# Optimization experiments

Hardware: AMD Instinct MI355X
Metric: run time of the kernel (lower is better)

## Reference

```python
import jax, jax.numpy as jnp
import numpy as np

N = 100000
E = 1600000
F = 128
H = 8
D = F // H
NC = 3


def setup_inputs() -> dict:
    key = jax.random.key(0)
    ks = jax.random.split(key, 12)
    s = lambda fan_in: 1.0 / np.sqrt(fan_in)
    x = jax.random.normal(ks[0], (N, F), dtype=jnp.float32)
    edge_index = jax.random.randint(ks[1], (2, E), 0, N, dtype=jnp.int64)
    edge_attr = jax.random.normal(ks[2], (E, 2), dtype=jnp.float32)
    # params stored as [in, out] so y = x @ W + b
    Wqkv = jax.random.uniform(ks[3], (F, 3 * F), jnp.float32, -s(F), s(F))
    Wedge = jax.random.uniform(ks[4], (2, H), jnp.float32, -s(2), s(2))
    Wout = jax.random.uniform(ks[5], (F, F), jnp.float32, -s(F), s(F))
    bout = jax.random.uniform(ks[6], (F,), jnp.float32, -s(F), s(F))
    ln_w = jnp.ones((F,), jnp.float32)
    ln_b = jnp.zeros((F,), jnp.float32)
    Wc1 = jax.random.uniform(ks[7], (F, F // 2), jnp.float32, -s(F), s(F))
    bc1 = jax.random.uniform(ks[8], (F // 2,), jnp.float32, -s(F), s(F))
    Wc2 = jax.random.uniform(ks[9], (F // 2, NC), jnp.float32, -s(F // 2), s(F // 2))
    bc2 = jax.random.uniform(ks[10], (NC,), jnp.float32, -s(F // 2), s(F // 2))
    return {"x": x, "edge_index": edge_index, "edge_attr": edge_attr,
            "Wqkv": Wqkv, "Wedge": Wedge, "Wout": Wout, "bout": bout,
            "ln_w": ln_w, "ln_b": ln_b,
            "Wc1": Wc1, "bc1": bc1, "Wc2": Wc2, "bc2": bc2}


def reference(x, edge_index, edge_attr, Wqkv, Wedge, Wout, bout,
              ln_w, ln_b, Wc1, bc1, Wc2, bc2):
    n = x.shape[0]
    scale = D ** (-0.5)
    qkv = x @ Wqkv                                # [N, 3F]
    q, k, v = [t.reshape(n, H, D) for t in jnp.split(qkv, 3, axis=-1)]
    src = edge_index[0]   # j (source / neighbor)
    dst = edge_index[1]   # i (target, softmax segment)
    edge_bias = edge_attr @ Wedge                 # [E, H]
    # per-edge biased attention score
    score = jnp.einsum('ehd,ehd->eh', q[dst], k[src]) * scale + edge_bias
    # segment softmax over incoming edges of each target node
    m = jax.lax.stop_gradient(jax.ops.segment_max(score, dst, num_segments=n))
    ex = jnp.exp(score - m[dst])
    denom = jax.ops.segment_sum(ex, dst, num_segments=n) + 1e-16
    w = ex / denom[dst]                           # [E, H]
    agg = jax.ops.segment_sum(v[src] * w[..., None], dst, num_segments=n)
    attn_out = agg.reshape(n, F) @ Wout + bout    # to_out
    h = x + attn_out
    mu = jnp.mean(h, axis=-1, keepdims=True)
    var = jnp.mean((h - mu) ** 2, axis=-1, keepdims=True)
    h = (h - mu) / jnp.sqrt(var + 1e-5) * ln_w + ln_b
    h = jax.nn.relu(h @ Wc1 + bc1)
    return h @ Wc2 + bc2
```

## Files before the change

kernel.cpp:

```cpp
#include <hip/hip_runtime.h>
#include <stdint.h>

#define N_NODES 100000
#define N_EDGES 1600000
#define FDIM 128
#define NH 8
#define NCLS 3

static constexpr float SCALE = 0.25f;

typedef _Float16 f16x8 __attribute__((ext_vector_type(8)));
typedef _Float16 f16x4 __attribute__((ext_vector_type(4)));
typedef float    f32x4 __attribute__((ext_vector_type(4)));

__global__ __launch_bounds__(256) void k_hist(const int* __restrict__ ei,
                                              int* __restrict__ cnt) {
    int e = blockIdx.x * 256 + threadIdx.x;
    if (e < N_EDGES) {
        int d = ei[N_EDGES + e];
        atomicAdd(&cnt[d], 1);
    }
}

__global__ __launch_bounds__(256) void k_scan1(const int* __restrict__ cnt,
                                               int* __restrict__ bsum) {
    __shared__ int sd[256];
    int t = threadIdx.x;
    int i0 = blockIdx.x * 1024 + t * 4;
    int s = 0;
#pragma unroll
    for (int j = 0; j < 4; ++j) {
        int i = i0 + j;
        if (i < N_NODES) s += cnt[i];
    }
    sd[t] = s;
    __syncthreads();
    for (int off = 128; off > 0; off >>= 1) {
        if (t < off) sd[t] += sd[t + off];
        __syncthreads();
    }
    if (t == 0) bsum[blockIdx.x] = sd[0];
}

__global__ __launch_bounds__(128) void k_scan2(const int* __restrict__ bsum,
                                               int* __restrict__ boff,
                                               int* __restrict__ row_start) {
    __shared__ int sd[128];
    int t = threadIdx.x;
    int v = (t < 98) ? bsum[t] : 0;
    sd[t] = v;
    __syncthreads();
    for (int off = 1; off < 128; off <<= 1) {
        int add = (t >= off) ? sd[t - off] : 0;
        __syncthreads();
        sd[t] += add;
        __syncthreads();
    }
    if (t < 98) boff[t] = sd[t] - v;
    if (t == 0) row_start[N_NODES] = N_EDGES;
}

__global__ __launch_bounds__(256) void k_scan3(const int* __restrict__ cnt,
                                               const int* __restrict__ boff,
                                               int* __restrict__ row_start,
                                               int* __restrict__ cursor) {
    __shared__ int sd[256];
    int t = threadIdx.x;
    int i0 = blockIdx.x * 1024 + t * 4;
    int c[4];
    int s = 0;
#pragma unroll
    for (int j = 0; j < 4; ++j) {
        int i = i0 + j;
        c[j] = (i < N_NODES) ? cnt[i] : 0;
        s += c[j];
    }
    sd[t] = s;
    __syncthreads();
    for (int off = 1; off < 256; off <<= 1) {
        int add = (t >= off) ? sd[t - off] : 0;
        __syncthreads();
        sd[t] += add;
        __syncthreads();
    }
    int run = boff[blockIdx.x] + sd[t] - s;
#pragma unroll
    for (int j = 0; j < 4; ++j) {
        int i = i0 + j;
        if (i < N_NODES) { row_start[i] = run; cursor[i] = run; }
        run += c[j];
    }
}

__global__ __launch_bounds__(256) void k_scatter(const int* __restrict__ ei,
                                                 const float* __restrict__ ea,
                                                 int* __restrict__ cursor,
                                                 float4* __restrict__ se4) {
    int e = blockIdx.x * 256 + threadIdx.x;
    if (e < N_EDGES) {
        int s = ei[e];
        int d = ei[N_EDGES + e];
        float2 a = *(const float2*)(ea + (long)e * 2);
        int pos = atomicAdd(&cursor[d], 1);
        se4[pos] = make_float4(__int_as_float(s), a.x, a.y, 0.0f);
    }
}

__global__ __launch_bounds__(256) void k_cvt(const float* __restrict__ x,
                                             const float* __restrict__ Wqkv,
                                             const float* __restrict__ Wout,
                                             _Float16* __restrict__ x_h,
                                             _Float16* __restrict__ Wqkv_t,
                                             _Float16* __restrict__ Wout_t) {
    long i = (long)blockIdx.x * 256 + threadIdx.x;
    float4 v = ((const float4*)x)[i];
    f16x4 h = { (_Float16)v.x, (_Float16)v.y, (_Float16)v.z, (_Float16)v.w };
    *(f16x4*)(x_h + i * 4) = h;
    if (i < 128 * 384) {
        int k = (int)(i / 384), n = (int)(i % 384);
        Wqkv_t[(long)n * 128 + k] = (_Float16)Wqkv[i];
    }
    if (i < 128 * 128) {
        int k = (int)(i / 128), n = (int)(i % 128);
        Wout_t[(long)n * 128 + k] = (_Float16)Wout[i];
    }
}

__global__ __launch_bounds__(256) void k_mm_qkv(const _Float16* __restrict__ x_h,
                                                const _Float16* __restrict__ Wt,
                                                float* __restrict__ q_tab,
                                                _Float16* __restrict__ kv_h) {
    int wave = threadIdx.x >> 6, l = threadIdx.x & 63;
    int row0 = blockIdx.x * 64 + wave * 16;
    int lr = l & 15, lg = l >> 4;
    int arow = row0 + lr;
    bool aok = arow < N_NODES;
    long abase = (long)arow * 128 + lg * 8;

    f32x4 acc[24];
#pragma unroll
    for (int c = 0; c < 24; ++c) acc[c] = (f32x4){0.f, 0.f, 0.f, 0.f};

#pragma unroll
    for (int kk = 0; kk < 4; ++kk) {
        f16x8 a = aok ? *(const f16x8*)(x_h + abase + kk * 32) : (f16x8){};
        const _Float16* wb = Wt + (long)lr * 128 + lg * 8 + kk * 32;
#pragma unroll
        for (int c = 0; c < 24; ++c) {
            f16x8 b = *(const f16x8*)(wb + (long)c * 16 * 128);
            acc[c] = __builtin_amdgcn_mfma_f32_16x16x32_f16(a, b, acc[c], 0, 0, 0);
        }
    }

    int orow_base = row0 + lg * 4;
#pragma unroll
    for (int c = 0; c < 24; ++c) {
#pragma unroll
        for (int j = 0; j < 4; ++j) {
            int orow = orow_base + j;
            if (orow < N_NODES) {
                float v = acc[c][j];
                if (c < 8)       q_tab[(long)orow * 128 + c * 16 + lr] = v;
                else if (c < 16) kv_h[(long)orow * 256 + (c - 8) * 16 + lr]        = (_Float16)v;
                else             kv_h[(long)orow * 256 + 128 + (c - 16) * 16 + lr] = (_Float16)v;
            }
        }
    }
}

__global__ __launch_bounds__(256) void k_mm_out(const _Float16* __restrict__ agg_h,
                                                const _Float16* __restrict__ Wot,
                                                const float* __restrict__ bout,
                                                const float* __restrict__ x,
                                                float* __restrict__ h_pre) {
    int wave = threadIdx.x >> 6, l = threadIdx.x & 63;
    int row0 = blockIdx.x * 64 + wave * 16;
    int lr = l & 15, lg = l >> 4;
    int arow = row0 + lr;
    bool aok = arow < N_NODES;
    long abase = (long)arow * 128 + lg * 8;

    f32x4 acc[8];
#pragma unroll
    for (int c = 0; c < 8; ++c) acc[c] = (f32x4){0.f, 0.f, 0.f, 0.f};

#pragma unroll
    for (int kk = 0; kk < 4; ++kk) {
        f16x8 a = aok ? *(const f16x8*)(agg_h + abase + kk * 32) : (f16x8){};
        const _Float16* wb = Wot + (long)lr * 128 + lg * 8 + kk * 32;
#pragma unroll
        for (int c = 0; c < 8; ++c) {
            f16x8 b = *(const f16x8*)(wb + (long)c * 16 * 128);
            acc[c] = __builtin_amdgcn_mfma_f32_16x16x32_f16(a, b, acc[c], 0, 0, 0);
        }
    }

    int orow_base = row0 + lg * 4;
#pragma unroll
    for (int c = 0; c < 8; ++c) {
        int ocol = c * 16 + lr;
        float bv = bout[ocol];
#pragma unroll
        for (int j = 0; j < 4; ++j) {
            int orow = orow_base + j;
            if (orow < N_NODES) {
                h_pre[(long)orow * 128 + ocol] = acc[c][j] + bv + x[(long)orow * 128 + ocol];
            }
        }
    }
}

__global__ __launch_bounds__(256) void k_attn(const float* __restrict__ q_tab,
                                              const _Float16* __restrict__ kv_tab,
                                              const float4* __restrict__ se4,
                                              const int* __restrict__ row_start,
                                              const float* __restrict__ Wedge,
                                              _Float16* __restrict__ agg_h) {
    int wave = threadIdx.x >> 6;
    int lane = threadIdx.x & 63;
    int node = blockIdx.x * 4 + wave;
    if (node >= N_NODES) return;

    int g  = lane >> 4;
    int gl = lane & 15;
    int h  = gl >> 1;

    int p0 = row_start[node], p1 = row_start[node + 1];
    if (p0 == p1) {
        if (g == 0) *(f16x8*)(agg_h + (long)node * 128 + gl * 8) = (f16x8){};
        return;
    }

    float we0 = Wedge[h];
    float we1 = Wedge[8 + h];
    const float* qb = q_tab + (long)node * 128 + gl * 8;
    float4 qa  = *(const float4*)(qb);
    float4 qbv = *(const float4*)(qb + 4);

    float a0=0.f,a1=0.f,a2=0.f,a3=0.f,a4=0.f,a5=0.f,a6=0.f,a7=0.f;
    float den = 0.f;

    int last = p1 - 1;
    float4 rec = se4[min(p0 + g, last)];
    for (int p = p0; p < p1; p += 4) {
        float4 cur = rec;
        int pn = p + 4;
        if (pn < p1) rec = se4[min(pn + g, last)];

        bool valid = (p + g) < p1;
        int src = __float_as_int(cur.x);
        const _Float16* kvb = kv_tab + (long)src * 256 + gl * 8;
        f16x8 kh = *(const f16x8*)(kvb);
        f16x8 vh = *(const f16x8*)(kvb + 128);

        float part = qa.x  * (float)kh[0] + qa.y  * (float)kh[1]
                   + qa.z  * (float)kh[2] + qa.w  * (float)kh[3]
                   + qbv.x * (float)kh[4] + qbv.y * (float)kh[5]
                   + qbv.z * (float)kh[6] + qbv.w * (float)kh[7];
        part += __shfl_xor(part, 1);

        float s = part * SCALE + cur.y * we0 + cur.z * we1;
        float w = valid ? __expf(s) : 0.f;
        den += w;
        a0 += w * (float)vh[0]; a1 += w * (float)vh[1];
        a2 += w * (float)vh[2]; a3 += w * (float)vh[3];
        a4 += w * (float)vh[4]; a5 += w * (float)vh[5];
        a6 += w * (float)vh[6]; a7 += w * (float)vh[7];
    }

#pragma unroll
    for (int off = 16; off <= 32; off <<= 1) {
        a0 += __shfl_xor(a0, off); a1 += __shfl_xor(a1, off);
        a2 += __shfl_xor(a2, off); a3 += __shfl_xor(a3, off);
        a4 += __shfl_xor(a4, off); a5 += __shfl_xor(a5, off);
        a6 += __shfl_xor(a6, off); a7 += __shfl_xor(a7, off);
        den += __shfl_xor(den, off);
    }

    if (g == 0) {
        float inv = 1.0f / (den + 1e-16f);
        f16x8 o = { (_Float16)(a0 * inv), (_Float16)(a1 * inv),
                    (_Float16)(a2 * inv), (_Float16)(a3 * inv),
                    (_Float16)(a4 * inv), (_Float16)(a5 * inv),
                    (_Float16)(a6 * inv), (_Float16)(a7 * inv) };
        *(f16x8*)(agg_h + (long)node * 128 + gl * 8) = o;
    }
}

__global__ __launch_bounds__(256) void k_mlp(const float* __restrict__ h_pre,
                                             const float* __restrict__ ln_w,
                                             const float* __restrict__ ln_b,
                                             const float* __restrict__ Wc1,
                                             const float* __restrict__ bc1,
                                             const float* __restrict__ Wc2,
                                             const float* __restrict__ bc2,
                                             float* __restrict__ out) {
    __shared__ float sW1[128 * 64];
    __shared__ float sW2[64 * 3];
    __shared__ float sb1[64];
    __shared__ float sb2[3];
    __shared__ float hbuf[4][4][128];
    int t = threadIdx.x;
#pragma unroll
    for (int it = 0; it < 8; ++it) {
        int f = (it * 256 + t) * 4;
        *(float4*)(sW1 + f) = *(const float4*)(Wc1 + f);
    }
    if (t < 192) sW2[t] = Wc2[t];
    if (t < 64) sb1[t] = bc1[t];
    if (t < 3) sb2[t] = bc2[t];
    __syncthreads();

    int wave = t >> 6, lane = t & 63;
    float2 lw = *(const float2*)(ln_w + lane * 2);
    float2 lb = *(const float2*)(ln_b + lane * 2);
    int nb0 = (blockIdx.x * 4 + wave) * 4;

#pragma unroll
    for (int nb = 0; nb < 4; ++nb) {
        int node = nb0 + nb;
        float2 hv = *(const float2*)(h_pre + (long)node * 128 + lane * 2);
        float s = hv.x + hv.y;
#pragma unroll
        for (int off = 32; off > 0; off >>= 1) s += __shfl_xor(s, off);
        float mu = s * (1.0f / 128.0f);
        float dx = hv.x - mu, dy = hv.y - mu;
        float s2 = dx * dx + dy * dy;
#pragma unroll
        for (int off = 32; off > 0; off >>= 1) s2 += __shfl_xor(s2, off);
        float rstd = rsqrtf(s2 * (1.0f / 128.0f) + 1e-5f);
        hbuf[wave][nb][lane * 2] = dx * rstd * lw.x + lb.x;
        hbuf[wave][nb][lane * 2 + 1] = dy * rstd * lw.y + lb.y;
    }
    __syncthreads();

    float acc[4];
#pragma unroll
    for (int nb = 0; nb < 4; ++nb) acc[nb] = sb1[lane];
#pragma unroll 4
    for (int c = 0; c < 128; ++c) {
        float w = sW1[c * 64 + lane];
        acc[0] += hbuf[wave][0][c] * w;
        acc[1] += hbuf[wave][1][c] * w;
        acc[2] += hbuf[wave][2][c] * w;
        acc[3] += hbuf[wave][3][c] * w;
    }
#pragma unroll
    for (int nb = 0; nb < 4; ++nb) {
        float a = fmaxf(acc[nb], 0.f);
#pragma unroll
        for (int c2 = 0; c2 < NCLS; ++c2) {
            float pv = a * sW2[lane * 3 + c2];
#pragma unroll
            for (int off = 32; off > 0; off >>= 1) pv += __shfl_xor(pv, off);
            if (lane == 0) out[(long)(nb0 + nb) * 3 + c2] = pv + sb2[c2];
        }
    }
}

extern "C" void kernel_launch(void* const* d_in, const int* in_sizes, int n_in,
                              void* d_out, int out_size, void* d_ws, size_t ws_size,
                              hipStream_t stream) {
    const float* x         = (const float*)d_in[0];
    const int*   edge_index= (const int*)d_in[1];
    const float* edge_attr = (const float*)d_in[2];
    const float* Wqkv      = (const float*)d_in[3];
    const float* Wedge     = (const float*)d_in[4];
    const float* Wout      = (const float*)d_in[5];
    const float* bout      = (const float*)d_in[6];
    const float* ln_w      = (const float*)d_in[7];
    const float* ln_b      = (const float*)d_in[8];
    const float* Wc1       = (const float*)d_in[9];
    const float* bc1       = (const float*)d_in[10];
    const float* Wc2       = (const float*)d_in[11];
    const float* bc2       = (const float*)d_in[12];
    float* out = (float*)d_out;

    char* ws = (char*)d_ws;
    size_t o = 0;
    auto alloc = [&](size_t bytes) -> char* {
        char* p = ws + o;
        o = (o + bytes + 255) & ~(size_t)255;
        return p;
    };
    int*       cnt       = (int*)alloc((size_t)N_NODES * 4);
    int*       row_start = (int*)alloc((size_t)(N_NODES + 1) * 4);
    int*       cursor    = (int*)alloc((size_t)N_NODES * 4);
    int*       bsum      = (int*)alloc(98 * 4);
    int*       boff      = (int*)alloc(98 * 4);
    float4*    se4       = (float4*)alloc((size_t)N_EDGES * 16);
    _Float16*  x_h       = (_Float16*)alloc((size_t)N_NODES * 128 * 2);
    _Float16*  Wqkv_t    = (_Float16*)alloc((size_t)384 * 128 * 2);
    _Float16*  Wout_t    = (_Float16*)alloc((size_t)128 * 128 * 2);
    float*     q_tab     = (float*)alloc((size_t)N_NODES * 128 * 4);
    _Float16*  kv_h      = (_Float16*)alloc((size_t)N_NODES * 256 * 2);
    _Float16*  agg_h     = (_Float16*)alloc((size_t)N_NODES * 128 * 2);
    float*     h_pre     = q_tab;
    (void)ws_size; (void)in_sizes; (void)n_in; (void)out_size;

    hipMemsetAsync(cnt, 0, (size_t)N_NODES * 4, stream);
    k_hist<<<N_EDGES / 256, 256, 0, stream>>>(edge_index, cnt);
    k_scan1<<<98, 256, 0, stream>>>(cnt, bsum);
    k_scan2<<<1, 128, 0, stream>>>(bsum, boff, row_start);
    k_scan3<<<98, 256, 0, stream>>>(cnt, boff, row_start, cursor);
    k_scatter<<<N_EDGES / 256, 256, 0, stream>>>(edge_index, edge_attr, cursor, se4);

    k_cvt<<<12500, 256, 0, stream>>>(x, Wqkv, Wout, x_h, Wqkv_t, Wout_t);
    k_mm_qkv<<<1563, 256, 0, stream>>>(x_h, Wqkv_t, q_tab, kv_h);
    k_attn<<<25000, 256, 0, stream>>>(q_tab, kv_h, se4, row_start, Wedge, agg_h);
    k_mm_out<<<1563, 256, 0, stream>>>(agg_h, Wout_t, bout, x, h_pre);
    k_mlp<<<6250, 256, 0, stream>>>(h_pre, ln_w, ln_b, Wc1, bc1, Wc2, bc2, out);
}
```

Baseline: 637.9 us.

## Build CSR via two-level bucketed binning instead of global atomic scatter

Replaces the global-atomic histogram and per-edge atomic cursor scatter with a two-pass radix-style binning. Edges are first grouped into coarse buckets of 128 destination nodes using shared-memory atomics, then each bucket is scattered to its final CSR position with shared-memory cursors. The goal is to cut contended global atomics and make the final scatter writes local within a small region. In exchange it adds an extra intermediate 1.6M×16B buffer pass and several more kernel launches.

```diff
diff --git a/kernel.cpp b/kernel.cpp
--- a/kernel.cpp
+++ b/kernel.cpp
@@ -6,6 +6,7 @@
 #define FDIM 128
 #define NH 8
 #define NCLS 3
+#define NB 782
 
 static constexpr float SCALE = 0.25f;
 
@@ -13,12 +14,87 @@
 typedef _Float16 f16x4 __attribute__((ext_vector_type(4)));
 typedef float    f32x4 __attribute__((ext_vector_type(4)));
 
-__global__ __launch_bounds__(256) void k_hist(const int* __restrict__ ei,
-                                              int* __restrict__ cnt) {
-    int e = blockIdx.x * 256 + threadIdx.x;
-    if (e < N_EDGES) {
-        int d = ei[N_EDGES + e];
-        atomicAdd(&cnt[d], 1);
+__global__ __launch_bounds__(256) void k_bhist(const int* __restrict__ ei,
+                                               int* __restrict__ bcnt) {
+    __shared__ int sb[NB];
+    for (int i = threadIdx.x; i < NB; i += 256) sb[i] = 0;
+    __syncthreads();
+    int e0 = blockIdx.x * 1024;
+#pragma unroll
+    for (int j = 0; j < 4; ++j) {
+        int e = e0 + j * 256 + threadIdx.x;
+        if (e < N_EDGES) atomicAdd(&sb[ei[N_EDGES + e] >> 7], 1);
+    }
+    __syncthreads();
+    for (int i = threadIdx.x; i < NB; i += 256)
+        if (sb[i]) atomicAdd(&bcnt[i], sb[i]);
+}
+
+__global__ __launch_bounds__(256) void k_bscan(const int* __restrict__ bcnt,
+                                               int* __restrict__ bbase,
+                                               int* __restrict__ bcur) {
+    __shared__ int sd[256];
+    int t = threadIdx.x;
+    int v[4]; int s = 0;
+#pragma unroll
+    for (int j = 0; j < 4; ++j) {
+        int i = t * 4 + j;
+        v[j] = (i < NB) ? bcnt[i] : 0;
+        s += v[j];
+    }
+    sd[t] = s;
+    __syncthreads();
+    for (int off = 1; off < 256; off <<= 1) {
+        int a = (t >= off) ? sd[t - off] : 0;
+        __syncthreads();
+        sd[t] += a;
+        __syncthreads();
+    }
+    int run = sd[t] - s;
+#pragma unroll
+    for (int j = 0; j < 4; ++j) {
+        int i = t * 4 + j;
+        if (i < NB) { bbase[i] = run; bcur[i] = run; }
+        run += v[j];
+    }
+    if (t == 0) bbase[NB] = N_EDGES;
+}
+
+__global__ __launch_bounds__(256) void k_bin(const int* __restrict__ ei,
+                                             const float* __restrict__ ea,
+                                             int* __restrict__ bcur,
+                                             int* __restrict__ cnt,
+                                             float4* __restrict__ binb) {
+    __shared__ int lcnt[NB];
+    __shared__ int lbase[NB];
+    for (int i = threadIdx.x; i < NB; i += 256) lcnt[i] = 0;
+    __syncthreads();
+    int e0 = blockIdx.x * 1024;
+    int rnk[4], bkt[4], src[4], dst[4];
+    float2 eav[4];
+#pragma unroll
+    for (int j = 0; j < 4; ++j) {
+        int e = e0 + j * 256 + threadIdx.x;
+        if (e < N_EDGES) {
+            src[j] = ei[e];
+            dst[j] = ei[N_EDGES + e];
+            eav[j] = *(const float2*)(ea + (long)e * 2);
+            bkt[j] = dst[j] >> 7;
+            rnk[j] = atomicAdd(&lcnt[bkt[j]], 1);
+            atomicAdd(&cnt[dst[j]], 1);
+        } else bkt[j] = -1;
+    }
+    __syncthreads();
+    for (int i = threadIdx.x; i < NB; i += 256)
+        if (lcnt[i]) lbase[i] = atomicAdd(&bcur[i], lcnt[i]);
+    __syncthreads();
+#pragma unroll
+    for (int j = 0; j < 4; ++j) {
+        if (bkt[j] >= 0) {
+            int pos = lbase[bkt[j]] + rnk[j];
+            binb[pos] = make_float4(__int_as_float(src[j]), __int_as_float(dst[j]),
+                                    eav[j].x, eav[j].y);
+        }
     }
 }
 
@@ -62,8 +138,7 @@
 
 __global__ __launch_bounds__(256) void k_scan3(const int* __restrict__ cnt,
                                                const int* __restrict__ boff,
-                                               int* __restrict__ row_start,
-                                               int* __restrict__ cursor) {
+                                               int* __restrict__ row_start) {
     __shared__ int sd[256];
     int t = threadIdx.x;
     int i0 = blockIdx.x * 1024 + t * 4;
@@ -87,22 +162,30 @@
 #pragma unroll
     for (int j = 0; j < 4; ++j) {
         int i = i0 + j;
-        if (i < N_NODES) { row_start[i] = run; cursor[i] = run; }
+        if (i < N_NODES) row_start[i] = run;
         run += c[j];
     }
 }
 
-__global__ __launch_bounds__(256) void k_scatter(const int* __restrict__ ei,
-                                                 const float* __restrict__ ea,
-                                                 int* __restrict__ cursor,
-                                                 float4* __restrict__ se4) {
-    int e = blockIdx.x * 256 + threadIdx.x;
-    if (e < N_EDGES) {
-        int s = ei[e];
-        int d = ei[N_EDGES + e];
-        float2 a = *(const float2*)(ea + (long)e * 2);
-        int pos = atomicAdd(&cursor[d], 1);
-        se4[pos] = make_float4(__int_as_float(s), a.x, a.y, 0.0f);
+__global__ __launch_bounds__(256) void k_fine(const float4* __restrict__ binb,
+                                              const int* __restrict__ bbase,
+                                              const int* __restrict__ row_start,
+                                              float4* __restrict__ se4) {
+    __shared__ int cur[128];
+    int b = blockIdx.x;
+    int n0 = b << 7;
+    int t = threadIdx.x;
+    if (t < 128) {
+        int n = n0 + t;
+        cur[t] = (n < N_NODES) ? row_start[n] : 0;
+    }
+    __syncthreads();
+    int p0 = bbase[b], p1 = bbase[b + 1];
+    for (int p = p0 + t; p < p1; p += 256) {
+        float4 r = binb[p];
+        int d = __float_as_int(r.y);
+        int pos = atomicAdd(&cur[d - n0], 1);
+        se4[pos] = make_float4(r.x, r.z, r.w, 0.f);
     }
 }
 
@@ -385,9 +468,12 @@
     };
     int*       cnt       = (int*)alloc((size_t)N_NODES * 4);
     int*       row_start = (int*)alloc((size_t)(N_NODES + 1) * 4);
-    int*       cursor    = (int*)alloc((size_t)N_NODES * 4);
     int*       bsum      = (int*)alloc(98 * 4);
     int*       boff      = (int*)alloc(98 * 4);
+    int*       bcnt      = (int*)alloc((size_t)NB * 4);
+    int*       bbase     = (int*)alloc((size_t)(NB + 1) * 4);
+    int*       bcur      = (int*)alloc((size_t)NB * 4);
+    float4*    binb      = (float4*)alloc((size_t)N_EDGES * 16);
     float4*    se4       = (float4*)alloc((size_t)N_EDGES * 16);
     _Float16*  x_h       = (_Float16*)alloc((size_t)N_NODES * 128 * 2);
     _Float16*  Wqkv_t    = (_Float16*)alloc((size_t)384 * 128 * 2);
@@ -399,11 +485,15 @@
     (void)ws_size; (void)in_sizes; (void)n_in; (void)out_size;
 
     hipMemsetAsync(cnt, 0, (size_t)N_NODES * 4, stream);
-    k_hist<<<N_EDGES / 256, 256, 0, stream>>>(edge_index, cnt);
+    hipMemsetAsync(bcnt, 0, (size_t)NB * 4, stream);
+
+    k_bhist<<<1563, 256, 0, stream>>>(edge_index, bcnt);
+    k_bscan<<<1, 256, 0, stream>>>(bcnt, bbase, bcur);
+    k_bin<<<1563, 256, 0, stream>>>(edge_index, edge_attr, bcur, cnt, binb);
     k_scan1<<<98, 256, 0, stream>>>(cnt, bsum);
     k_scan2<<<1, 128, 0, stream>>>(bsum, boff, row_start);
-    k_scan3<<<98, 256, 0, stream>>>(cnt, boff, row_start, cursor);
-    k_scatter<<<N_EDGES / 256, 256, 0, stream>>>(edge_index, edge_attr, cursor, se4);
+    k_scan3<<<98, 256, 0, stream>>>(cnt, boff, row_start);
+    k_fine<<<NB, 256, 0, stream>>>(binb, bbase, row_start, se4);
 
     k_cvt<<<12500, 256, 0, stream>>>(x, Wqkv, Wout, x_h, Wqkv_t, Wout_t);
     k_mm_qkv<<<1563, 256, 0, stream>>>(x_h, Wqkv_t, q_tab, kv_h);
```

Result: no change. 646.7 us (+1.4%).
